# Performance work log

Measured on AMD Instinct MI355X. Metric: run time of the kernel, lower is better.

## Reference

```python
import jax, jax.numpy as jnp
import numpy as np

D, H, O, NEXP, NA = 128, 256, 128, 8, 5  # na = max(1, int(8*0.7)) = 5
T = float(np.e)  # gate temperature
N_TOKENS = 131072


def ternary_quantize(w):
    # per-expert-matrix threshold: alpha = mean(|W|) over each [out,in] matrix
    alpha = jnp.mean(jnp.abs(w), axis=(-2, -1), keepdims=True)
    return jnp.sign(w) * (jnp.abs(w) > 0.5 * alpha).astype(w.dtype)


def setup_inputs() -> dict:
    key = jax.random.key(0)
    ks = jax.random.split(key, 7)
    x = jax.random.normal(ks[0], (N_TOKENS, D), dtype=jnp.float32)
    # expert params stacked over expert dim e (nn.Linear layout: [out, in])
    w1 = jax.random.normal(ks[1], (NEXP, H, D), dtype=jnp.float32) * 0.05
    b1 = jax.random.normal(ks[2], (NEXP, H), dtype=jnp.float32) * 0.05
    w2 = jax.random.normal(ks[3], (NEXP, O, H), dtype=jnp.float32) * 0.05
    b2 = jax.random.normal(ks[4], (NEXP, O), dtype=jnp.float32) * 0.05
    wg = jax.random.normal(ks[5], (NEXP, D), dtype=jnp.float32) * 0.05
    bg = jax.random.normal(ks[6], (NEXP,), dtype=jnp.float32) * 0.05
    return {"x": x, "w1": w1, "b1": b1, "w2": w2, "b2": b2, "wg": wg, "bg": bg}


def reference(x, w1, b1, w2, b2, wg, bg):
    # Ternary-quantize expert weights on the fly (TW.forward); dropout in eval mode (identity).
    w1q = ternary_quantize(w1)
    w2q = ternary_quantize(w2)
    # all-expert dense MLP: x [t,d] -> hidden [t,e,h] -> eo [t,e,o]
    hid = jax.nn.relu(jnp.einsum('td,ehd->teh', x, w1q) + b1[None, :, :])
    eo = jnp.einsum('teh,eoh->teo', hid, w2q) + b2[None, :, :]
    # BG gate: tempered softmax, top-k mask, renormalize
    p = jax.nn.softmax((x @ wg.T + bg) / T, axis=-1)          # [t,e]
    _, idx = jax.lax.top_k(p, NA)                             # [t,na]
    m = jnp.sum(jax.nn.one_hot(idx, NEXP, dtype=p.dtype), axis=-2)  # [t,e] 0/1 mask
    w = p * m
    w = w / (jnp.sum(w, axis=-1, keepdims=True) + 1e-8)
    return jnp.einsum('te,teo->to', w, eo)
```

## Files before the change

kernel.cpp:

```cpp
#include <hip/hip_runtime.h>
#include <hip/hip_bf16.h>

typedef unsigned int u32;
typedef unsigned char u8;
typedef unsigned short u16;
using f32x4  = __attribute__((ext_vector_type(4))) float;
using f32x16 = __attribute__((ext_vector_type(16))) float;
using u32x4  = __attribute__((ext_vector_type(4))) u32;
using s16x8  = __attribute__((ext_vector_type(8))) short;

#define DEV static __device__ __forceinline__

DEV u32 pk2(float a, float b) {
  u16 lo = __builtin_bit_cast(u16, __float2bfloat16(a));
  u16 hi = __builtin_bit_cast(u16, __float2bfloat16(b));
  return (u32)lo | ((u32)hi << 16);
}

DEV f32x16 MFMA32(u32x4 a, u32x4 b, f32x16 c) {
  return __builtin_amdgcn_mfma_f32_32x32x16_bf16(
      __builtin_bit_cast(s16x8, a), __builtin_bit_cast(s16x8, b), c, 0, 0, 0);
}

DEV void pl32swap(u32& a, u32& b) {
  asm volatile("v_permlane32_swap_b32 %0, %1" : "+v"(a), "+v"(b));
}

typedef const __attribute__((address_space(1))) u32 gu32;
typedef __attribute__((address_space(3))) u32 lu32;

DEV void load_lds16(const void* g, void* l) {
  __builtin_amdgcn_global_load_lds((gu32*)g, (lu32*)l, 16, 0, 0);
}

DEV u16 tq1(float v, float thr) {
  return (fabsf(v) > thr) ? (v > 0.f ? (u16)0x3F80 : (u16)0xBF80) : (u16)0;
}
DEV u32 tq2(float a, float b, float thr) {
  return (u32)tq1(a, thr) | ((u32)tq1(b, thr) << 16);
}

__global__ void k_alpha(const float* __restrict__ w1, const float* __restrict__ w2,
                        float* __restrict__ alphas, uint4* __restrict__ histz) {
  int b = blockIdx.x;
  int tid = threadIdx.x;
  histz[b * 256 + tid] = make_uint4(0, 0, 0, 0);
  const float* src = (b < 8 ? w1 : w2) + (size_t)(b & 7) * 32768;
  float s = 0.f;
  for (int i = tid; i < 32768; i += 256) s += fabsf(src[i]);
  #pragma unroll
  for (int off = 32; off >= 1; off >>= 1) s += __shfl_down(s, off, 64);
  __shared__ float ws4[4];
  if ((tid & 63) == 0) ws4[tid >> 6] = s;
  __syncthreads();
  if (tid == 0) alphas[b] = (ws4[0] + ws4[1] + ws4[2] + ws4[3]) * (1.f / 32768.f);
}

__global__ void k_img_gate(const float* __restrict__ w1,
                           const float* __restrict__ w2,
                           const float* __restrict__ alphas,
                           char* __restrict__ img, const float* __restrict__ x,
                           const float* __restrict__ wg,
                           const float* __restrict__ bg, float* __restrict__ gw,
                           u8* __restrict__ maskA, u32* __restrict__ hist) {
  const int tid = threadIdx.x;
  if (blockIdx.x < 256) {
    int gid = blockIdx.x * 256 + tid;
    int l = gid & 63;
    int col = l & 31, hi = l >> 5;
    const float* src;
    float thr;
    char* dst;
    if (gid < 32768) {
      int ks = (gid >> 6) & 7;
      int n  = gid >> 9;
      int e  = n >> 3, ht = n & 7;
      int h  = ht * 32 + col;
      int k0 = ks * 16 + hi * 8;
      src = w1 + (size_t)e * 32768 + h * 128 + k0;
      thr = 0.5f * alphas[e];
      dst = img + (size_t)n * 16384 + ks * 1024 + l * 16;
    } else {
      int id = gid - 32768;
      int sl = (id >> 6) & 7;
      int n  = id >> 9;
      int e  = n >> 3, c = n & 7;
      int ks2 = sl >> 2, ot = sl & 3;
      int o  = ot * 32 + col;
      int k0 = c * 32 + ks2 * 16 + hi * 8;
      src = w2 + (size_t)e * 32768 + o * 256 + k0;
      thr = 0.5f * alphas[8 + e];
      dst = img + (size_t)n * 16384 + 8192 + sl * 1024 + l * 16;
    }
    float4 v0 = *(const float4*)src;
    float4 v1 = *(const float4*)(src + 4);
    *(uint4*)dst = make_uint4(tq2(v0.x, v0.y, thr), tq2(v0.z, v0.w, thr),
                              tq2(v1.x, v1.y, thr), tq2(v1.z, v1.w, thr));
    return;
  }
  __shared__ float s_wg[1024];
  __shared__ float s_bg[8];
  __shared__ u32 lh[256];
  ((float4*)s_wg)[tid] = ((const float4*)wg)[tid];
  if (tid < 8) s_bg[tid] = bg[tid];
  lh[tid] = 0;
  __syncthreads();

  int t = (blockIdx.x - 256) * 256 + tid;
  const float4* xr = (const float4*)(x + (size_t)t * 128);
  float lg[8];
  #pragma unroll
  for (int e = 0; e < 8; ++e) lg[e] = s_bg[e];
  for (int i = 0; i < 32; ++i) {
    float4 xv = xr[i];
    #pragma unroll
    for (int e = 0; e < 8; ++e) {
      f32x4 wv = *(const f32x4*)(s_wg + e * 128 + i * 4);
      lg[e] += xv.x * wv.x + xv.y * wv.y + xv.z * wv.z + xv.w * wv.w;
    }
  }
  const float invT = 0.36787944117144233f;
  #pragma unroll
  for (int e = 0; e < 8; ++e) lg[e] *= invT;
  float mx = lg[0];
  #pragma unroll
  for (int e = 1; e < 8; ++e) mx = fmaxf(mx, lg[e]);
  float p[8], den = 0.f;
  #pragma unroll
  for (int e = 0; e < 8; ++e) { p[e] = __expf(lg[e] - mx); den += p[e]; }
  float inv = 1.f / den;
  #pragma unroll
  for (int e = 0; e < 8; ++e) p[e] *= inv;
  float gsel[8], wsum = 0.f;
  u32 m = 0;
  #pragma unroll
  for (int e = 0; e < 8; ++e) {
    int rank = 0;
    #pragma unroll
    for (int e2 = 0; e2 < 8; ++e2)
      rank += (p[e2] > p[e]) || (p[e2] == p[e] && e2 < e);
    bool sel = rank < 5;
    if (sel) m |= 1u << e;
    gsel[e] = sel ? p[e] : 0.f;
    wsum += gsel[e];
  }
  float r = 1.f / (wsum + 1e-8f);
  float* gwp = gw + (size_t)t * 8;
  *(f32x4*)gwp       = (f32x4){gsel[0] * r, gsel[1] * r, gsel[2] * r, gsel[3] * r};
  *(f32x4*)(gwp + 4) = (f32x4){gsel[4] * r, gsel[5] * r, gsel[6] * r, gsel[7] * r};
  maskA[t] = (u8)m;
  __syncthreads();
  atomicAdd(&lh[m], 1u);
  __syncthreads();
  if (lh[tid]) atomicAdd(&hist[tid << 5], lh[tid]);
}

__global__ void k_scatter(const u32* __restrict__ hist, const u8* __restrict__ maskA,
                          u32* __restrict__ cur2, u32* __restrict__ perm) {
  __shared__ u32 s[256], lh[256], lb[256];
  const int t = threadIdx.x;
  u32 h = hist[t << 5];
  s[t] = h;
  lh[t] = 0;
  __syncthreads();
  #pragma unroll
  for (int o = 1; o < 256; o <<= 1) {
    u32 v = (t >= o) ? s[t - o] : 0u;
    __syncthreads();
    s[t] += v;
    __syncthreads();
  }
  const u32 pbase = s[t] - h;
  int tkn = blockIdx.x * 256 + t;
  u32 m = maskA[tkn];
  u32 r = atomicAdd(&lh[m], 1u);
  __syncthreads();
  if (lh[t]) lb[t] = pbase + atomicAdd(&cur2[t << 5], lh[t]);
  __syncthreads();
  perm[lb[m] + r] = (u32)tkn;
}

#define B1_OFF 65536
#define G_OFF  73728
#define SMEM_BYTES 81920

__global__ __launch_bounds__(256, 2) void moe_main(
    const float* __restrict__ x, const float* __restrict__ b1g,
    const float* __restrict__ b2g, const char* __restrict__ img,
    const u32* __restrict__ perm, const u8* __restrict__ maskA,
    const float* __restrict__ gw, float* __restrict__ out) {
  extern __shared__ char smem[];
  float* s_b1 = (float*)(smem + B1_OFF);
  float* s_g  = (float*)(smem + G_OFF);
  u32*   s_u  = (u32*)(smem + G_OFF);
  const int tid = threadIdx.x;
  const int w = tid >> 6, l = tid & 63;
  const int col = l & 31, hi = l >> 5;
  const int base = blockIdx.x * 256;
  const u32 loff = (u32)(l * 16);

  {
    const u32 ptg = perm[base + tid];
    s_u[tid] = (u32)maskA[ptg];
  }
  __syncthreads();
  #pragma unroll
  for (int st = 128; st >= 1; st >>= 1) {
    if (tid < st) s_u[tid] |= s_u[tid + st];
    __syncthreads();
  }
  const u32 bmask = __builtin_amdgcn_readfirstlane(s_u[0]);
  __syncthreads();

  u32 elist = 0;
  int cnt = 0;
  #pragma unroll
  for (int e = 0; e < 8; ++e)
    if ((bmask >> e) & 1) { elist |= (u32)e << (4 * cnt); ++cnt; }
  elist = __builtin_amdgcn_readfirstlane(elist);
  const int iters = __builtin_amdgcn_readfirstlane(cnt * 4);

  auto stage_pair = [&](int P, int slot) {
    const char* src = img + (size_t)P * 32768 + w * 8192 + loff;
    char* dst = smem + slot * 32768 + w * 8192;
    #pragma unroll
    for (int i = 0; i < 8; ++i)
      load_lds16(src + i * 1024, dst + i * 1024);
  };

  stage_pair((elist & 7) * 4, 0);

  u32x4 xf[2][8];
  {
    const u32 ptg = perm[base + tid];
    f32x4 gA = *(const f32x4*)(gw + (size_t)ptg * 8);
    f32x4 gB = *(const f32x4*)(gw + (size_t)ptg * 8 + 4);
    s_g[0 * 256 + tid] = gA.x; s_g[1 * 256 + tid] = gA.y;
    s_g[2 * 256 + tid] = gA.z; s_g[3 * 256 + tid] = gA.w;
    s_g[4 * 256 + tid] = gB.x; s_g[5 * 256 + tid] = gB.y;
    s_g[6 * 256 + tid] = gB.z; s_g[7 * 256 + tid] = gB.w;
    const float4* s = (const float4*)b1g;
    float4* d = (float4*)s_b1;
    d[tid] = s[tid];
    d[tid + 256] = s[tid + 256];

    #pragma unroll
    for (int tt = 0; tt < 2; ++tt) {
      const u32 pt = perm[base + w * 64 + tt * 32 + col];
      #pragma unroll
      for (int ks = 0; ks < 8; ++ks) {
        const float* xp = x + (size_t)pt * 128 + ks * 16 + hi * 8;
        float4 v0 = *(const float4*)xp;
        float4 v1 = *(const float4*)(xp + 4);
        xf[tt][ks] = (u32x4){pk2(v0.x, v0.y), pk2(v0.z, v0.w),
                             pk2(v1.x, v1.y), pk2(v1.z, v1.w)};
      }
    }
  }
  __syncthreads();

  f32x16 acc2[4][2];
  {
    u32x4 gf[2];
    #pragma unroll
    for (int tt = 0; tt < 2; ++tt) {
      u32x4 v = (u32x4){0u, 0u, 0u, 0u};
      if (hi == 0) {
        int t = w * 64 + tt * 32 + col;
        v = (u32x4){pk2(s_g[0 * 256 + t], s_g[1 * 256 + t]),
                    pk2(s_g[2 * 256 + t], s_g[3 * 256 + t]),
                    pk2(s_g[4 * 256 + t], s_g[5 * 256 + t]),
                    pk2(s_g[6 * 256 + t], s_g[7 * 256 + t])};
      }
      gf[tt] = v;
    }
    #pragma unroll
    for (int ot = 0; ot < 4; ++ot) {
      u32x4 af = (u32x4){0u, 0u, 0u, 0u};
      if (hi == 0) {
        int o = ot * 32 + col;
        af = (u32x4){pk2(b2g[0 * 128 + o], b2g[1 * 128 + o]),
                     pk2(b2g[2 * 128 + o], b2g[3 * 128 + o]),
                     pk2(b2g[4 * 128 + o], b2g[5 * 128 + o]),
                     pk2(b2g[6 * 128 + o], b2g[7 * 128 + o])};
      }
      f32x16 z{};
      #pragma unroll
      for (int tt = 0; tt < 2; ++tt) acc2[ot][tt] = MFMA32(af, gf[tt], z);
    }
  }

  auto chunk = [&](const char* cb, int e, int ht, float g0, float g1) {
    f32x16 a1_0{}, a1_1{};
    __builtin_amdgcn_s_setprio(1);
    #pragma unroll
    for (int ks = 0; ks < 8; ++ks) {
      u32x4 f = *(const u32x4*)(cb + ks * 1024 + loff);
      a1_0 = MFMA32(f, xf[0][ks], a1_0);
      a1_1 = MFMA32(f, xf[1][ks], a1_1);
    }
    __builtin_amdgcn_s_setprio(0);

    const float* b1b = s_b1 + e * 256 + ht * 32 + hi * 4;
    u32x4 hf[2][2];
    #pragma unroll
    for (int tt = 0; tt < 2; ++tt) {
      const f32x16& a1 = tt ? a1_1 : a1_0;
      const float g = tt ? g1 : g0;
      u32 u[8];
      #pragma unroll
      for (int rg = 0; rg < 4; ++rg) {
        f32x4 bb = *(const f32x4*)(b1b + rg * 8);
        float h0 = fmaxf(a1[rg * 4 + 0] + bb.x, 0.f) * g;
        float h1 = fmaxf(a1[rg * 4 + 1] + bb.y, 0.f) * g;
        float h2 = fmaxf(a1[rg * 4 + 2] + bb.z, 0.f) * g;
        float h3 = fmaxf(a1[rg * 4 + 3] + bb.w, 0.f) * g;
        u[rg * 2 + 0] = pk2(h0, h1);
        u[rg * 2 + 1] = pk2(h2, h3);
      }
      pl32swap(u[0], u[2]);
      pl32swap(u[1], u[3]);
      pl32swap(u[4], u[6]);
      pl32swap(u[5], u[7]);
      hf[0][tt] = (u32x4){u[0], u[1], u[2], u[3]};
      hf[1][tt] = (u32x4){u[4], u[5], u[6], u[7]};
    }

    __builtin_amdgcn_s_setprio(1);
    #pragma unroll
    for (int ks2 = 0; ks2 < 2; ++ks2) {
      #pragma unroll
      for (int ot = 0; ot < 4; ++ot) {
        u32x4 af = *(const u32x4*)(cb + 8192 + (ks2 * 4 + ot) * 1024 + loff);
        acc2[ot][0] = MFMA32(af, hf[ks2][0], acc2[ot][0]);
        acc2[ot][1] = MFMA32(af, hf[ks2][1], acc2[ot][1]);
      }
    }
    __builtin_amdgcn_s_setprio(0);
  };

  #pragma unroll 1
  for (int i = 0; i < iters; ++i) {
    asm volatile("s_waitcnt vmcnt(0)" ::: "memory");
    __builtin_amdgcn_s_barrier();
    __builtin_amdgcn_sched_barrier(0);
    if (i + 1 < iters) {
      const int j = i + 1;
      const int ej = (elist >> (4 * (j >> 2))) & 7;
      stage_pair(ej * 4 + (j & 3), j & 1);
    }
    const int ei = (elist >> (4 * (i >> 2))) & 7;
    const int ht0 = (i & 3) * 2;
    const float g0 = s_g[ei * 256 + w * 64 + col];
    const float g1 = s_g[ei * 256 + w * 64 + 32 + col];
    const char* buf = smem + (i & 1) * 32768;
    chunk(buf, ei, ht0, g0, g1);
    __builtin_amdgcn_sched_barrier(0);
    chunk(buf + 16384, ei, ht0 + 1, g0, g1);
  }

  #pragma unroll
  for (int tt = 0; tt < 2; ++tt) {
    const u32 pt = perm[base + w * 64 + tt * 32 + col];
    #pragma unroll
    for (int ot = 0; ot < 4; ++ot) {
      const f32x16& a = acc2[ot][tt];
      float* op = out + (size_t)pt * 128 + ot * 32 + hi * 4;
      #pragma unroll
      for (int rg = 0; rg < 4; ++rg)
        *(f32x4*)(op + rg * 8) =
            (f32x4){a[rg * 4 + 0], a[rg * 4 + 1], a[rg * 4 + 2], a[rg * 4 + 3]};
    }
  }
}

extern "C" void kernel_launch(void* const* d_in, const int* in_sizes, int n_in,
                              void* d_out, int out_size, void* d_ws, size_t ws_size,
                              hipStream_t stream) {
  const float* x  = (const float*)d_in[0];
  const float* w1 = (const float*)d_in[1];
  const float* b1 = (const float*)d_in[2];
  const float* w2 = (const float*)d_in[3];
  const float* b2 = (const float*)d_in[4];
  const float* wg = (const float*)d_in[5];
  const float* bg = (const float*)d_in[6];
  float* out = (float*)d_out;

  int ntok = in_sizes[0] / 128;
  int nblk = ntok / 256;

  char* ws = (char*)d_ws;
  char*  img    = ws;
  float* alphas = (float*)(ws + 1048576);
  u32*   hist   = (u32*)(ws + 1048640);
  u32*   cur2   = (u32*)(ws + 1081408);
  u8*    maskA  = (u8*)(ws + 1114176);
  u32*   perm   = (u32*)(ws + 1245248);
  float* gw     = (float*)(ws + 1769536);
  if (ws_size < 5963840) return;

  k_alpha<<<16, 256, 0, stream>>>(w1, w2, alphas, (uint4*)hist);
  k_img_gate<<<256 + nblk, 256, 0, stream>>>(w1, w2, alphas, img, x, wg, bg,
                                             gw, maskA, hist);
  k_scatter<<<nblk, 256, 0, stream>>>(hist, maskA, cur2, perm);

  hipFuncSetAttribute(reinterpret_cast<const void*>(moe_main),
                      hipFuncAttributeMaxDynamicSharedMemorySize, SMEM_BYTES);
  moe_main<<<nblk, 256, SMEM_BYTES, stream>>>(x, b1, b2, img, perm, maskA, gw,
                                              out);
}
```

Before: 186.2 us.

## Fuse alpha into weight-image kernel and schedule MoE blocks by expert count

Drops the separate alpha kernel. Each weight-image block now recomputes its matrix's mean-abs threshold itself, and the histogram is zeroed with a memset instead. An extra block in the scatter kernel works out each 256-token tile's union expert mask from the prefix sums. It then orders the tiles by how many experts they use, interleaving heavy and light tiles. This removes the per-block mask reduction in the main kernel and is meant to balance its load. The cost is redundant threshold reductions, one block for every 2K elements, and an ordering step that assumes 512 token blocks.

```diff
diff --git a/kernel.cpp b/kernel.cpp
--- a/kernel.cpp
+++ b/kernel.cpp
@@ -40,36 +40,36 @@
   return (u32)tq1(a, thr) | ((u32)tq1(b, thr) << 16);
 }
 
-__global__ void k_alpha(const float* __restrict__ w1, const float* __restrict__ w2,
-                        float* __restrict__ alphas, uint4* __restrict__ histz) {
-  int b = blockIdx.x;
-  int tid = threadIdx.x;
-  histz[b * 256 + tid] = make_uint4(0, 0, 0, 0);
-  const float* src = (b < 8 ? w1 : w2) + (size_t)(b & 7) * 32768;
-  float s = 0.f;
-  for (int i = tid; i < 32768; i += 256) s += fabsf(src[i]);
-  #pragma unroll
-  for (int off = 32; off >= 1; off >>= 1) s += __shfl_down(s, off, 64);
-  __shared__ float ws4[4];
-  if ((tid & 63) == 0) ws4[tid >> 6] = s;
-  __syncthreads();
-  if (tid == 0) alphas[b] = (ws4[0] + ws4[1] + ws4[2] + ws4[3]) * (1.f / 32768.f);
-}
-
 __global__ void k_img_gate(const float* __restrict__ w1,
                            const float* __restrict__ w2,
-                           const float* __restrict__ alphas,
                            char* __restrict__ img, const float* __restrict__ x,
                            const float* __restrict__ wg,
                            const float* __restrict__ bg, float* __restrict__ gw,
                            u8* __restrict__ maskA, u32* __restrict__ hist) {
   const int tid = threadIdx.x;
   if (blockIdx.x < 256) {
-    int gid = blockIdx.x * 256 + tid;
+    const int b = blockIdx.x;
+    const float* wsrc = (b < 128) ? (w1 + (size_t)(b >> 4) * 32768)
+                                  : (w2 + (size_t)((b - 128) >> 4) * 32768);
+    float s = 0.f;
+    const float4* wv4 = (const float4*)wsrc;
+    #pragma unroll
+    for (int j = 0; j < 32; ++j) {
+      float4 v = wv4[tid + j * 256];
+      s += fabsf(v.x) + fabsf(v.y) + fabsf(v.z) + fabsf(v.w);
+    }
+    #pragma unroll
+    for (int off = 32; off >= 1; off >>= 1) s += __shfl_down(s, off, 64);
+    __shared__ float ws4[4];
+    if ((tid & 63) == 0) ws4[tid >> 6] = s;
+    __syncthreads();
+    const float thr =
+        0.5f * (ws4[0] + ws4[1] + ws4[2] + ws4[3]) * (1.f / 32768.f);
+
+    int gid = b * 256 + tid;
     int l = gid & 63;
     int col = l & 31, hi = l >> 5;
     const float* src;
-    float thr;
     char* dst;
     if (gid < 32768) {
       int ks = (gid >> 6) & 7;
@@ -78,7 +78,6 @@
       int h  = ht * 32 + col;
       int k0 = ks * 16 + hi * 8;
       src = w1 + (size_t)e * 32768 + h * 128 + k0;
-      thr = 0.5f * alphas[e];
       dst = img + (size_t)n * 16384 + ks * 1024 + l * 16;
     } else {
       int id = gid - 32768;
@@ -89,7 +88,6 @@
       int o  = ot * 32 + col;
       int k0 = c * 32 + ks2 * 16 + hi * 8;
       src = w2 + (size_t)e * 32768 + o * 256 + k0;
-      thr = 0.5f * alphas[8 + e];
       dst = img + (size_t)n * 16384 + 8192 + sl * 1024 + l * 16;
     }
     float4 v0 = *(const float4*)src;
@@ -156,28 +154,80 @@
 }
 
 __global__ void k_scatter(const u32* __restrict__ hist, const u8* __restrict__ maskA,
-                          u32* __restrict__ cur2, u32* __restrict__ perm) {
-  __shared__ u32 s[256], lh[256], lb[256];
+                          u32* __restrict__ cur2, u32* __restrict__ perm,
+                          u32* __restrict__ order, u32* __restrict__ umask) {
   const int t = threadIdx.x;
+  if (blockIdx.x < 512) {
+    __shared__ u32 s[256], lh[256], lb[256];
+    u32 h = hist[t << 5];
+    s[t] = h;
+    lh[t] = 0;
+    __syncthreads();
+    #pragma unroll
+    for (int o = 1; o < 256; o <<= 1) {
+      u32 v = (t >= o) ? s[t - o] : 0u;
+      __syncthreads();
+      s[t] += v;
+      __syncthreads();
+    }
+    const u32 pbase = s[t] - h;
+    int tkn = blockIdx.x * 256 + t;
+    u32 m = maskA[tkn];
+    u32 r = atomicAdd(&lh[m], 1u);
+    __syncthreads();
+    if (lh[t]) lb[t] = pbase + atomicAdd(&cur2[t << 5], lh[t]);
+    __syncthreads();
+    perm[lb[m] + r] = (u32)tkn;
+    return;
+  }
+  __shared__ u32 sh[256], sA[256], spfx[256];
+  __shared__ u32 bcnt[4], bcur[4], boff[4];
+  __shared__ u32 L[512];
   u32 h = hist[t << 5];
-  s[t] = h;
-  lh[t] = 0;
+  sh[t] = h;
+  sA[t] = h;
+  if (t < 4) { bcnt[t] = 0; bcur[t] = 0; }
   __syncthreads();
   #pragma unroll
   for (int o = 1; o < 256; o <<= 1) {
-    u32 v = (t >= o) ? s[t - o] : 0u;
-    __syncthreads();
-    s[t] += v;
-    __syncthreads();
-  }
-  const u32 pbase = s[t] - h;
-  int tkn = blockIdx.x * 256 + t;
-  u32 m = maskA[tkn];
-  u32 r = atomicAdd(&lh[m], 1u);
-  __syncthreads();
-  if (lh[t]) lb[t] = pbase + atomicAdd(&cur2[t << 5], lh[t]);
-  __syncthreads();
-  perm[lb[m] + r] = (u32)tkn;
+    u32 v = (t >= o) ? sA[t - o] : 0u;
+    __syncthreads();
+    sA[t] += v;
+    __syncthreads();
+  }
+  spfx[t] = sA[t] - h;
+  __syncthreads();
+  int c[2];
+  int mb[2] = {t, t + 256};
+  #pragma unroll
+  for (int k = 0; k < 2; ++k) {
+    u32 start = (u32)mb[k] * 256u, end = start + 256u;
+    u32 un = 0;
+    for (int m = 0; m < 256; ++m) {
+      u32 p0 = spfx[m];
+      if (sh[m] && p0 < end && p0 + sh[m] > start) un |= (u32)m;
+    }
+    umask[mb[k]] = un;
+    c[k] = (int)__popc(un);
+    atomicAdd(&bcnt[8 - c[k]], 1);
+  }
+  __syncthreads();
+  if (t == 0) {
+    boff[0] = 0;
+    boff[1] = bcnt[0];
+    boff[2] = bcnt[0] + bcnt[1];
+    boff[3] = bcnt[0] + bcnt[1] + bcnt[2];
+  }
+  __syncthreads();
+  #pragma unroll
+  for (int k = 0; k < 2; ++k) {
+    int q = 8 - c[k];
+    u32 pos = boff[q] + atomicAdd(&bcur[q], 1);
+    L[pos] = (u32)mb[k];
+  }
+  __syncthreads();
+  order[2 * t]     = L[t];
+  order[2 * t + 1] = L[511 - t];
 }
 
 #define B1_OFF 65536
@@ -187,31 +237,20 @@
 __global__ __launch_bounds__(256, 2) void moe_main(
     const float* __restrict__ x, const float* __restrict__ b1g,
     const float* __restrict__ b2g, const char* __restrict__ img,
-    const u32* __restrict__ perm, const u8* __restrict__ maskA,
-    const float* __restrict__ gw, float* __restrict__ out) {
+    const u32* __restrict__ perm, const float* __restrict__ gw,
+    const u32* __restrict__ order, const u32* __restrict__ umask,
+    float* __restrict__ out) {
   extern __shared__ char smem[];
   float* s_b1 = (float*)(smem + B1_OFF);
   float* s_g  = (float*)(smem + G_OFF);
-  u32*   s_u  = (u32*)(smem + G_OFF);
   const int tid = threadIdx.x;
   const int w = tid >> 6, l = tid & 63;
   const int col = l & 31, hi = l >> 5;
-  const int base = blockIdx.x * 256;
+  const int bid = (int)order[blockIdx.x];
+  const int base = bid * 256;
   const u32 loff = (u32)(l * 16);
 
-  {
-    const u32 ptg = perm[base + tid];
-    s_u[tid] = (u32)maskA[ptg];
-  }
-  __syncthreads();
-  #pragma unroll
-  for (int st = 128; st >= 1; st >>= 1) {
-    if (tid < st) s_u[tid] |= s_u[tid + st];
-    __syncthreads();
-  }
-  const u32 bmask = __builtin_amdgcn_readfirstlane(s_u[0]);
-  __syncthreads();
-
+  const u32 bmask = __builtin_amdgcn_readfirstlane(umask[bid]);
   u32 elist = 0;
   int cnt = 0;
   #pragma unroll
@@ -391,21 +430,22 @@
 
   char* ws = (char*)d_ws;
   char*  img    = ws;
-  float* alphas = (float*)(ws + 1048576);
-  u32*   hist   = (u32*)(ws + 1048640);
-  u32*   cur2   = (u32*)(ws + 1081408);
-  u8*    maskA  = (u8*)(ws + 1114176);
-  u32*   perm   = (u32*)(ws + 1245248);
-  float* gw     = (float*)(ws + 1769536);
-  if (ws_size < 5963840) return;
-
-  k_alpha<<<16, 256, 0, stream>>>(w1, w2, alphas, (uint4*)hist);
-  k_img_gate<<<256 + nblk, 256, 0, stream>>>(w1, w2, alphas, img, x, wg, bg,
+  u32*   hist   = (u32*)(ws + 1048576);
+  u32*   cur2   = (u32*)(ws + 1081344);
+  u32*   order  = (u32*)(ws + 1114112);
+  u32*   umask  = (u32*)(ws + 1116160);
+  u8*    maskA  = (u8*)(ws + 1118208);
+  u32*   perm   = (u32*)(ws + 1249280);
+  float* gw     = (float*)(ws + 1773568);
+  if (ws_size < 5967872) return;
+
+  hipMemsetAsync(hist, 0, 65536, stream);
+  k_img_gate<<<256 + nblk, 256, 0, stream>>>(w1, w2, img, x, wg, bg,
                                              gw, maskA, hist);
-  k_scatter<<<nblk, 256, 0, stream>>>(hist, maskA, cur2, perm);
+  k_scatter<<<nblk + 1, 256, 0, stream>>>(hist, maskA, cur2, perm, order, umask);
 
   hipFuncSetAttribute(reinterpret_cast<const void*>(moe_main),
                       hipFuncAttributeMaxDynamicSharedMemorySize, SMEM_BYTES);
-  moe_main<<<nblk, 256, SMEM_BYTES, stream>>>(x, b1, b2, img, perm, maskA, gw,
-                                              out);
-}
+  moe_main<<<nblk, 256, SMEM_BYTES, stream>>>(x, b1, b2, img, perm, gw,
+                                              order, umask, out);
+}
```

New measurement: 162.3 us. -12.8%, faster.
